# Optimization experiments

Hardware: AMD Instinct MI355X
Metric: run time of the kernel (lower is better)

Reference implementation:

```python
import jax, jax.numpy as jnp
import numpy as np

EPS = 1e-6
DATA_DIM = 2048
LATENT_DIM = 64
ENC = [1024, 1024, 2048]
BATCH = 8192
K_ROUNDS = 24  # fixed proposal rounds for Marsaglia-Tsang rejection (accept prob per round > 0.95)


def _sample_gamma_boosted(key, al, be):
    """Marsaglia-Tsang sampler with alpha-boost, matching the torch al<1 branch.

    Samples Gamma(al+1, 1) via squeeze/rejection, then applies the
    u^(1/al) boost and divides by be, exactly as:
    exp(log(d*v + 1e-6) + log(u + 1e-6)/(al + 1e-6)) / (be + 1e-6)
    """
    d = (al + 1.0) - 1.0 / 3.0              # [B, L]
    c = 1.0 / jnp.sqrt(9.0 * d)             # [B, L]
    k1, k2 = jax.random.split(key)
    eps = jax.random.normal(k1, (K_ROUNDS,) + al.shape, dtype=al.dtype)
    u = jax.random.uniform(k2, (K_ROUNDS,) + al.shape, dtype=al.dtype,
                           minval=1e-7, maxval=1.0)
    v = 1.0 + c[None] * eps                 # [K, B, L]
    v3 = v * v * v
    safe_v3 = jnp.where(v > 0, v3, 1.0)
    # squeeze accept OR full log-accept (standard MT test, as in source index1/index2)
    accept = (v > 0) & ((u < 1.0 - 0.0331 * (eps * eps) * (eps * eps)) |
                        (jnp.log(u) < 0.5 * eps * eps + d[None] * (1.0 - safe_v3 + jnp.log(safe_v3))))
    idx = jnp.argmax(accept, axis=0)        # first accepted round per element
    eps_s = jnp.take_along_axis(eps, idx[None], axis=0)[0]
    u_s = jnp.take_along_axis(u, idx[None], axis=0)[0]
    v_s = (1.0 + c * eps_s) ** 3
    return jnp.exp(jnp.log(d * v_s + EPS) + jnp.log(u_s + EPS) / (al + EPS)) / (be + EPS)


def setup_inputs() -> dict:
    key = jax.random.key(0)
    ks = jax.random.split(key, 20)

    def lin(k, fan_in, fan_out):
        kw, kb = jax.random.split(k)
        w = jax.random.normal(kw, (fan_in, fan_out), dtype=jnp.float32) / np.sqrt(fan_in)
        b = jax.random.normal(kb, (fan_out,), dtype=jnp.float32) * 0.01
        return w, b

    inp = {"x": jax.random.uniform(ks[0], (BATCH, DATA_DIM), dtype=jnp.float32)}
    inp["fc1_w"], inp["fc1_b"] = lin(ks[1], DATA_DIM, ENC[0])
    inp["fc2_w"], inp["fc2_b"] = lin(ks[2], ENC[0], ENC[1])
    inp["fc3_w"], inp["fc3_b"] = lin(ks[3], ENC[1], ENC[2])
    inp["fc41_w"], inp["fc41_b"] = lin(ks[4], ENC[2], LATENT_DIM)
    inp["fc42_w"], inp["fc42_b"] = lin(ks[5], ENC[2], LATENT_DIM)
    inp["fc4_w"], inp["fc4_b"] = lin(ks[6], LATENT_DIM, ENC[2])
    inp["fc5_w"], inp["fc5_b"] = lin(ks[7], ENC[2], ENC[1])
    inp["fc6_w"], inp["fc6_b"] = lin(ks[8], ENC[1], ENC[0])
    inp["fc7_w"], inp["fc7_b"] = lin(ks[9], ENC[0], DATA_DIM * 2)
    return inp


def reference(x, fc1_w, fc1_b, fc2_w, fc2_b, fc3_w, fc3_b,
              fc41_w, fc41_b, fc42_w, fc42_b,
              fc4_w, fc4_b, fc5_w, fc5_b, fc6_w, fc6_b, fc7_w, fc7_b):
    relu, sp = jax.nn.relu, jax.nn.softplus
    # encoder
    h1 = relu(x @ fc1_w + fc1_b)
    h2 = relu(h1 @ fc2_w + fc2_b)
    h3 = relu(h2 @ fc3_w + fc3_b)
    logalpha = EPS + sp(h3 @ fc41_w + fc41_b)   # [B, L], positive
    logbeta = EPS + sp(h3 @ fc42_w + fc42_b)
    # reparameterize via Marsaglia-Tsang gamma rejection sampling
    z = _sample_gamma_boosted(jax.random.key(42), logalpha, logbeta)
    # decoder (torch calls decode(z) twice with identical result; compute once)
    h4 = relu(z @ fc4_w + fc4_b)
    h5 = relu(h4 @ fc5_w + fc5_b)
    h6 = relu(h5 @ fc6_w + fc6_b)
    dec = h6 @ fc7_w + fc7_b                    # [B, 2*DATA_DIM]
    recon_al = EPS + sp(dec[:, :DATA_DIM])
    recon_be = EPS + sp(dec[:, DATA_DIM:])
    return (recon_al, recon_be, logalpha, logbeta, z)
```

## Files before the change

### kernel.cpp

```cpp
#include <hip/hip_runtime.h>
#include <stdint.h>

#define DEVFN static __device__ __forceinline__

typedef __attribute__((ext_vector_type(8))) short short8;
typedef __attribute__((ext_vector_type(4))) float floatx4;
typedef _Float16 half8 __attribute__((ext_vector_type(8)));

DEVFN uint32_t rotl32(uint32_t v, int d) { return (v << d) | (v >> (32 - d)); }

DEVFN void tf2x32(uint32_t k0, uint32_t k1, uint32_t x0, uint32_t x1,
                  uint32_t& o0, uint32_t& o1) {
  uint32_t k2 = k0 ^ k1 ^ 0x1BD11BDAu;
  x0 += k0; x1 += k1;
  x0 += x1; x1 = rotl32(x1, 13); x1 ^= x0;
  x0 += x1; x1 = rotl32(x1, 15); x1 ^= x0;
  x0 += x1; x1 = rotl32(x1, 26); x1 ^= x0;
  x0 += x1; x1 = rotl32(x1, 6);  x1 ^= x0;
  x0 += k1; x1 += k2 + 1u;
  x0 += x1; x1 = rotl32(x1, 17); x1 ^= x0;
  x0 += x1; x1 = rotl32(x1, 29); x1 ^= x0;
  x0 += x1; x1 = rotl32(x1, 16); x1 ^= x0;
  x0 += x1; x1 = rotl32(x1, 24); x1 ^= x0;
  x0 += k2; x1 += k0 + 2u;
  x0 += x1; x1 = rotl32(x1, 13); x1 ^= x0;
  x0 += x1; x1 = rotl32(x1, 15); x1 ^= x0;
  x0 += x1; x1 = rotl32(x1, 26); x1 ^= x0;
  x0 += x1; x1 = rotl32(x1, 6);  x1 ^= x0;
  x0 += k0; x1 += k1 + 3u;
  x0 += x1; x1 = rotl32(x1, 17); x1 ^= x0;
  x0 += x1; x1 = rotl32(x1, 29); x1 ^= x0;
  x0 += x1; x1 = rotl32(x1, 16); x1 ^= x0;
  x0 += x1; x1 = rotl32(x1, 24); x1 ^= x0;
  x0 += k1; x1 += k2 + 4u;
  x0 += x1; x1 = rotl32(x1, 13); x1 ^= x0;
  x0 += x1; x1 = rotl32(x1, 15); x1 ^= x0;
  x0 += x1; x1 = rotl32(x1, 26); x1 ^= x0;
  x0 += x1; x1 = rotl32(x1, 6);  x1 ^= x0;
  x0 += k2; x1 += k0 + 5u;
  o0 = x0; o1 = x1;
}

DEVFN float erfinv_f32(float x) {
#pragma clang fp contract(off)
  float w = -log1pf(-(x * x));
  float p;
  if (w < 5.0f) {
    w = w - 2.5f;
    p = 2.81022636e-08f;
    p = 3.43273939e-07f + p * w;
    p = -3.5233877e-06f + p * w;
    p = -4.39150654e-06f + p * w;
    p = 0.00021858087f + p * w;
    p = -0.00125372503f + p * w;
    p = -0.00417768164f + p * w;
    p = 0.246640727f + p * w;
    p = 1.50140941f + p * w;
  } else {
    w = __fsqrt_rn(w) - 3.0f;
    p = -0.000200214257f;
    p = 0.000100950558f + p * w;
    p = 0.00134934322f + p * w;
    p = -0.00367342844f + p * w;
    p = 0.00573950773f + p * w;
    p = -0.0076224613f + p * w;
    p = 0.00943887047f + p * w;
    p = 1.00167406f + p * w;
    p = 2.83297682f + p * w;
  }
  return p * x;
}

DEVFN float softplus_ref(float v) {
#pragma clang fp contract(off)
  return fmaxf(v, 0.0f) + log1pf(expf(-fabsf(v)));
}

DEVFN float softplus_fast(float v) {
  float e = __expf(-fabsf(v));
  return fmaxf(v, 0.0f) + __logf(1.0f + e);
}

DEVFN ushort f2bf(float f) {
  uint32_t u = __float_as_uint(f);
  uint32_t r = (u + 0x7FFFu + ((u >> 16) & 1u)) >> 16;
  return (ushort)r;
}

DEVFN void split2(float a, ushort& hb, ushort& lb) {
  _Float16 h = (_Float16)a;
  float r = (a - (float)h) * 2048.0f;
  _Float16 l = (_Float16)r;
  hb = __builtin_bit_cast(unsigned short, h);
  lb = __builtin_bit_cast(unsigned short, l);
}

DEVFN void gl2lds16(const void* g, void* l) {
  __builtin_amdgcn_global_load_lds(
      (const __attribute__((address_space(1))) void*)g,
      (__attribute__((address_space(3))) void*)l, 16, 0, 0);
}

DEVFN int xcd_swizzle(int bid, int nwg) {
  if ((nwg & 7) == 0) return (bid & 7) * (nwg >> 3) + (bid >> 3);
  return bid;
}

__global__ __launch_bounds__(256) void split_f16(
    const float* __restrict__ in, ushort* __restrict__ oh,
    ushort* __restrict__ ol, int n4) {
  int idx = blockIdx.x * 256 + threadIdx.x;
  int stride = gridDim.x * 256;
  for (int i = idx; i < n4; i += stride) {
    float4 a = ((const float4*)in)[i];
    ushort h0, h1, h2, h3, l0, l1, l2, l3;
    split2(a.x, h0, l0); split2(a.y, h1, l1);
    split2(a.z, h2, l2); split2(a.w, h3, l3);
    ushort4 hv; hv.x = h0; hv.y = h1; hv.z = h2; hv.w = h3;
    ushort4 lv; lv.x = l0; lv.y = l1; lv.z = l2; lv.w = l3;
    ((ushort4*)oh)[i] = hv;
    ((ushort4*)ol)[i] = lv;
  }
}

__global__ __launch_bounds__(256) void transpose_split_f16(
    const float* __restrict__ in, ushort* __restrict__ oh,
    ushort* __restrict__ ol, int R, int C) {
  __shared__ float tile[32][33];
  const int c0 = blockIdx.x * 32, r0 = blockIdx.y * 32;
  const int tx = threadIdx.x & 31, ty = threadIdx.x >> 5;
#pragma unroll
  for (int i = ty; i < 32; i += 8)
    tile[i][tx] = in[(size_t)(r0 + i) * C + c0 + tx];
  __syncthreads();
#pragma unroll
  for (int i = ty; i < 32; i += 8) {
    ushort hb, lb;
    split2(tile[tx][i], hb, lb);
    size_t o = (size_t)(c0 + i) * R + r0 + tx;
    oh[o] = hb; ol[o] = lb;
  }
}

template <int ACT>
__global__ __launch_bounds__(256) void gemm_f16x3(
    const ushort* __restrict__ Ah, const ushort* __restrict__ Al,
    const ushort* __restrict__ Bh, const ushort* __restrict__ Bl,
    const float* __restrict__ bias, ushort* __restrict__ Oh,
    ushort* __restrict__ Ol, float* __restrict__ Of, int M, int N, int K) {
  __shared__ ushort AsH[2][128 * 32];
  __shared__ ushort AsL[2][128 * 32];
  __shared__ ushort BsH[2][128 * 32];
  __shared__ ushort BsL[2][128 * 32];
  const int tid = threadIdx.x;
  const int wave = tid >> 6, lane = tid & 63;
  const int nbx = gridDim.x;
  const int bid = xcd_swizzle(blockIdx.y * nbx + blockIdx.x, nbx * gridDim.y);
  const int m0 = (bid / nbx) * 128, n0 = (bid % nbx) * 128;
  const int lrow = lane & 15, lq = lane >> 4;
  const int wm = wave & 1, wn = wave >> 1;
  const int srow = lane >> 2;
  const int scol = (lane & 3) * 8;

  floatx4 acc1[4][4], acc2[4][4];
#pragma unroll
  for (int i = 0; i < 4; i++)
#pragma unroll
    for (int j = 0; j < 4; j++) {
      acc1[i][j] = (floatx4){0.f, 0.f, 0.f, 0.f};
      acc2[i][j] = (floatx4){0.f, 0.f, 0.f, 0.f};
    }

  auto stage = [&](int k0, int pp) {
#pragma unroll
    for (int h = 0; h < 2; h++) {
      int r0 = wave * 32 + h * 16;
      gl2lds16(Ah + (size_t)(m0 + r0 + srow) * K + k0 + scol, &AsH[pp][r0 * 32]);
      gl2lds16(Al + (size_t)(m0 + r0 + srow) * K + k0 + scol, &AsL[pp][r0 * 32]);
      gl2lds16(Bh + (size_t)(n0 + r0 + srow) * K + k0 + scol, &BsH[pp][r0 * 32]);
      gl2lds16(Bl + (size_t)(n0 + r0 + srow) * K + k0 + scol, &BsL[pp][r0 * 32]);
    }
  };

  const int nt = K >> 5;
  stage(0, 0);
  int cur = 0;
  for (int t = 0; t < nt; t++) {
    if (t + 1 < nt) {
      stage((t + 1) << 5, cur ^ 1);
      asm volatile("s_waitcnt vmcnt(8)" ::: "memory");
    } else {
      asm volatile("s_waitcnt vmcnt(0)" ::: "memory");
    }
    __builtin_amdgcn_sched_barrier(0);
    __builtin_amdgcn_s_barrier();
    __builtin_amdgcn_sched_barrier(0);
    half8 ah[4], al[4];
#pragma unroll
    for (int i = 0; i < 4; i++) {
      ah[i] = *(const half8*)&AsH[cur][(wm * 64 + i * 16 + lrow) * 32 + lq * 8];
      al[i] = *(const half8*)&AsL[cur][(wm * 64 + i * 16 + lrow) * 32 + lq * 8];
    }
#pragma unroll
    for (int j = 0; j < 4; j++) {
      half8 bh = *(const half8*)&BsH[cur][(wn * 64 + j * 16 + lrow) * 32 + lq * 8];
      half8 bl = *(const half8*)&BsL[cur][(wn * 64 + j * 16 + lrow) * 32 + lq * 8];
#pragma unroll
      for (int i = 0; i < 4; i++) {
        acc1[i][j] = __builtin_amdgcn_mfma_f32_16x16x32_f16(ah[i], bh,
                                                            acc1[i][j], 0, 0, 0);
        acc2[i][j] = __builtin_amdgcn_mfma_f32_16x16x32_f16(ah[i], bl,
                                                            acc2[i][j], 0, 0, 0);
        acc2[i][j] = __builtin_amdgcn_mfma_f32_16x16x32_f16(al[i], bh,
                                                            acc2[i][j], 0, 0, 0);
      }
    }
    __builtin_amdgcn_sched_barrier(0);
    __builtin_amdgcn_s_barrier();
    __builtin_amdgcn_sched_barrier(0);
    cur ^= 1;
  }

  const float INV2048 = 4.8828125e-4f;
#pragma unroll
  for (int i = 0; i < 4; i++) {
#pragma unroll
    for (int j = 0; j < 4; j++) {
      int colg = n0 + wn * 64 + j * 16 + lrow;
      float bb = bias[colg];
#pragma unroll
      for (int r = 0; r < 4; r++) {
        int rowg = m0 + wm * 64 + i * 16 + lq * 4 + r;
        float v = acc1[i][j][r] + acc2[i][j][r] * INV2048 + bb;
        v = fmaxf(v, 0.0f);
        if (ACT == 1) {
          ushort hb, lb;
          split2(v, hb, lb);
          size_t o = (size_t)rowg * N + colg;
          Oh[o] = hb; Ol[o] = lb;
        } else {
          Of[(size_t)rowg * N + colg] = v;
        }
      }
    }
  }
}

__global__ __launch_bounds__(256) void dual_mfma(
    const ushort* __restrict__ Ah, const ushort* __restrict__ Al,
    const ushort* __restrict__ Bh, const ushort* __restrict__ Bl,
    float* __restrict__ P) {
  __shared__ ushort AsH[128 * 32];
  __shared__ ushort AsL[128 * 32];
  __shared__ ushort BsH[128 * 32];
  __shared__ ushort BsL[128 * 32];
  const int K = 2048;
  const int tid = threadIdx.x;
  const int wave = tid >> 6, lane = tid & 63;
  const int m0 = blockIdx.y * 128;
  const int kbase = blockIdx.x * 256;
  const int lrow = lane & 15, lq = lane >> 4;
  const int wm = wave & 1, wn = wave >> 1;
  const int srow = lane >> 2;
  const int scol = (lane & 3) * 8;

  floatx4 acc1[4][4], acc2[4][4];
#pragma unroll
  for (int i = 0; i < 4; i++)
#pragma unroll
    for (int j = 0; j < 4; j++) {
      acc1[i][j] = (floatx4){0.f, 0.f, 0.f, 0.f};
      acc2[i][j] = (floatx4){0.f, 0.f, 0.f, 0.f};
    }

  for (int kk = 0; kk < 256; kk += 32) {
    int k0 = kbase + kk;
#pragma unroll
    for (int h = 0; h < 2; h++) {
      int r0 = wave * 32 + h * 16;
      gl2lds16(Ah + (size_t)(m0 + r0 + srow) * K + k0 + scol, &AsH[r0 * 32]);
      gl2lds16(Al + (size_t)(m0 + r0 + srow) * K + k0 + scol, &AsL[r0 * 32]);
      gl2lds16(Bh + (size_t)(r0 + srow) * K + k0 + scol, &BsH[r0 * 32]);
      gl2lds16(Bl + (size_t)(r0 + srow) * K + k0 + scol, &BsL[r0 * 32]);
    }
    __syncthreads();
    half8 ah[4], al[4];
#pragma unroll
    for (int i = 0; i < 4; i++) {
      ah[i] = *(const half8*)&AsH[(wm * 64 + i * 16 + lrow) * 32 + lq * 8];
      al[i] = *(const half8*)&AsL[(wm * 64 + i * 16 + lrow) * 32 + lq * 8];
    }
#pragma unroll
    for (int j = 0; j < 4; j++) {
      half8 bh = *(const half8*)&BsH[(wn * 64 + j * 16 + lrow) * 32 + lq * 8];
      half8 bl = *(const half8*)&BsL[(wn * 64 + j * 16 + lrow) * 32 + lq * 8];
#pragma unroll
      for (int i = 0; i < 4; i++) {
        acc1[i][j] = __builtin_amdgcn_mfma_f32_16x16x32_f16(ah[i], bh,
                                                            acc1[i][j], 0, 0, 0);
        acc2[i][j] = __builtin_amdgcn_mfma_f32_16x16x32_f16(ah[i], bl,
                                                            acc2[i][j], 0, 0, 0);
        acc2[i][j] = __builtin_amdgcn_mfma_f32_16x16x32_f16(al[i], bh,
                                                            acc2[i][j], 0, 0, 0);
      }
    }
    __syncthreads();
  }

  const float INV2048 = 4.8828125e-4f;
#pragma unroll
  for (int i = 0; i < 4; i++) {
#pragma unroll
    for (int j = 0; j < 4; j++) {
      int colg = wn * 64 + j * 16 + lrow;
#pragma unroll
      for (int r = 0; r < 4; r++) {
        int rowg = m0 + wm * 64 + i * 16 + lq * 4 + r;
        float v = acc1[i][j][r] + acc2[i][j][r] * INV2048;
        P[((size_t)blockIdx.x * 8192 + rowg) * 128 + colg] = v;
      }
    }
  }
}

__global__ __launch_bounds__(256) void dual_reduce(
    const float* __restrict__ P, const float* __restrict__ b41,
    const float* __restrict__ b42, float* __restrict__ la,
    float* __restrict__ lb) {
#pragma clang fp contract(off)
  int idx = blockIdx.x * 256 + threadIdx.x;
  int row = idx >> 5;
  int c4 = (idx & 31) * 4;
  float4 s = {0.f, 0.f, 0.f, 0.f};
#pragma unroll
  for (int k = 0; k < 8; k++) {
    float4 p = *(const float4*)&P[((size_t)k * 8192 + row) * 128 + c4];
    s.x += p.x; s.y += p.y; s.z += p.z; s.w += p.w;
  }
  float o[4];
  const float* bb = (c4 < 64) ? (b41 + c4) : (b42 + c4 - 64);
#pragma unroll
  for (int q = 0; q < 4; q++) {
    float v = (&s.x)[q] + bb[q];
    o[q] = 1e-6f + softplus_ref(v);
  }
  float* dst = (c4 < 64) ? (la + (size_t)row * 64 + c4)
                         : (lb + (size_t)row * 64 + (c4 - 64));
  *(float4*)dst = *(float4*)o;
}

__global__ __launch_bounds__(256) void gamma_sampler(
    const float* __restrict__ la, const float* __restrict__ lb,
    float* __restrict__ z, ushort* __restrict__ zb) {
#pragma clang fp contract(off)
  const uint32_t i = blockIdx.x * 256u + threadIdx.x;
  uint32_t k1a, k1b, k2a, k2b;
  tf2x32(0u, 42u, 0u, 0u, k1a, k1b);
  tf2x32(0u, 42u, 0u, 1u, k2a, k2b);

  const float LO = __uint_as_float(0xBF7FFFFFu);
  const float SQRT2 = __uint_as_float(0x3FB504F3u);
  const float USCALE = 1.0f - 1e-7f;

  const float al = la[i];
  const float be = lb[i];
  const float d = (al + 1.0f) - 0.33333334f;
  const float c = 1.0f / __fsqrt_rn(9.0f * d);

  float es = 0.0f, us = 0.0f;
  bool done = false;
  for (int k = 0; k < 24; k++) {
    if (__all(done)) break;
    if (!done) {
      uint32_t n = (uint32_t)k * 524288u + i;
      uint32_t o0, o1, p0, p1;
      tf2x32(k1a, k1b, 0u, n, o0, o1);
      tf2x32(k2a, k2b, 0u, n, p0, p1);
      uint32_t eb = o0 ^ o1;
      uint32_t ub = p0 ^ p1;
      float f = __uint_as_float((eb >> 9) | 0x3F800000u) - 1.0f;
      float un = f * 2.0f + LO;
      un = fmaxf(LO, un);
      float e = SQRT2 * erfinv_f32(un);
      float g = __uint_as_float((ub >> 9) | 0x3F800000u) - 1.0f;
      float u = g * USCALE + 1e-7f;
      u = fmaxf(1e-7f, u);
      if (k == 0) { es = e; us = u; }
      float v = 1.0f + c * e;
      if (v > 0.0f) {
        float v3 = (v * v) * v;
        float e2 = e * e;
        bool acc = false;
        float sq = 1.0f - (0.0331f * e2) * e2;
        if (u < sq) acc = true;
        else {
          float rhs = (0.5f * e) * e + d * ((1.0f - v3) + logf(v3));
          if (logf(u) < rhs) acc = true;
        }
        if (acc) { es = e; us = u; done = true; }
      }
    }
  }
  float vv = 1.0f + c * es;
  float vs = (vv * vv) * vv;
  float t = logf(d * vs + 1e-6f) + logf(us + 1e-6f) / (al + 1e-6f);
  float zv = expf(t) / (be + 1e-6f);
  z[i] = zv;
  zb[i] = f2bf(zv);
}

__global__ __launch_bounds__(256) void transpose_bf16(
    const float* __restrict__ in, ushort* __restrict__ out, int R, int C) {
  __shared__ float tile[32][33];
  const int c0 = blockIdx.x * 32, r0 = blockIdx.y * 32;
  const int tx = threadIdx.x & 31, ty = threadIdx.x >> 5;
#pragma unroll
  for (int i = ty; i < 32; i += 8)
    tile[i][tx] = in[(size_t)(r0 + i) * C + c0 + tx];
  __syncthreads();
#pragma unroll
  for (int i = ty; i < 32; i += 8)
    out[(size_t)(c0 + i) * R + r0 + tx] = f2bf(tile[tx][i]);
}

template <int ACT>
__global__ __launch_bounds__(256) void gemm_bf16(
    const ushort* __restrict__ A, const ushort* __restrict__ Bt,
    const float* __restrict__ bias, ushort* __restrict__ C0b,
    float* __restrict__ C0f, float* __restrict__ C1f,
    int M, int N, int K, int split) {
  __shared__ ushort As[3][128 * 32];
  __shared__ ushort Bs[3][128 * 32];
  const int tid = threadIdx.x;
  const int wave = tid >> 6, lane = tid & 63;
  const int nbx = gridDim.x;
  const int bid = xcd_swizzle(blockIdx.y * nbx + blockIdx.x, nbx * gridDim.y);
  const int m0 = (bid / nbx) * 128, n0 = (bid % nbx) * 128;
  const int lrow = lane & 15, lq = lane >> 4;
  const int wm = wave & 1, wn = wave >> 1;
  const int srow = lane >> 2;
  const int scol = (lane & 3) * 8;

  floatx4 acc[4][4];
#pragma unroll
  for (int i = 0; i < 4; i++)
#pragma unroll
    for (int j = 0; j < 4; j++) acc[i][j] = (floatx4){0.f, 0.f, 0.f, 0.f};

  auto stage = [&](int k0, int pp) {
#pragma unroll
    for (int h = 0; h < 2; h++) {
      int r0 = wave * 32 + h * 16;
      gl2lds16(A + (size_t)(m0 + r0 + srow) * K + k0 + scol, &As[pp][r0 * 32]);
      gl2lds16(Bt + (size_t)(n0 + r0 + srow) * K + k0 + scol, &Bs[pp][r0 * 32]);
    }
  };

  const int nt = K >> 5;
  stage(0, 0);
  stage(32, 1);
  int cur = 0;
  for (int t = 0; t < nt; t++) {
    if (t + 2 < nt) {
      int nb = cur + 2; if (nb >= 3) nb -= 3;
      stage((t + 2) << 5, nb);
      asm volatile("s_waitcnt vmcnt(8)" ::: "memory");
    } else if (t + 1 < nt) {
      asm volatile("s_waitcnt vmcnt(4)" ::: "memory");
    } else {
      asm volatile("s_waitcnt vmcnt(0)" ::: "memory");
    }
    __builtin_amdgcn_sched_barrier(0);
    __builtin_amdgcn_s_barrier();
    __builtin_amdgcn_sched_barrier(0);
    short8 a[4], b[4];
#pragma unroll
    for (int i = 0; i < 4; i++) {
      a[i] = *(const short8*)&As[cur][(wm * 64 + i * 16 + lrow) * 32 + lq * 8];
      b[i] = *(const short8*)&Bs[cur][(wn * 64 + i * 16 + lrow) * 32 + lq * 8];
    }
#pragma unroll
    for (int i = 0; i < 4; i++)
#pragma unroll
      for (int j = 0; j < 4; j++)
        acc[i][j] = __builtin_amdgcn_mfma_f32_16x16x32_bf16(a[i], b[j],
                                                            acc[i][j], 0, 0, 0);
    __builtin_amdgcn_sched_barrier(0);
    __builtin_amdgcn_s_barrier();
    __builtin_amdgcn_sched_barrier(0);
    cur = cur + 1; if (cur == 3) cur = 0;
  }

#pragma unroll
  for (int i = 0; i < 4; i++) {
#pragma unroll
    for (int j = 0; j < 4; j++) {
      int colg = n0 + wn * 64 + j * 16 + lrow;
      float bb = bias[colg];
#pragma unroll
      for (int r = 0; r < 4; r++) {
        int rowg = m0 + wm * 64 + i * 16 + lq * 4 + r;
        float v = acc[i][j][r] + bb;
        if (ACT == 0) {
          v = fmaxf(v, 0.0f);
          C0b[(size_t)rowg * N + colg] = f2bf(v);
        } else {
          v = 1e-6f + softplus_fast(v);
          if (colg < split) C0f[(size_t)rowg * split + colg] = v;
          else              C1f[(size_t)rowg * split + (colg - split)] = v;
        }
      }
    }
  }
}

extern "C" void kernel_launch(void* const* d_in, const int* in_sizes, int n_in,
                              void* d_out, int out_size, void* d_ws,
                              size_t ws_size, hipStream_t stream) {
  const float* x   = (const float*)d_in[0];
  const float* w1  = (const float*)d_in[1];  const float* b1  = (const float*)d_in[2];
  const float* w2  = (const float*)d_in[3];  const float* b2  = (const float*)d_in[4];
  const float* w3  = (const float*)d_in[5];  const float* b3  = (const float*)d_in[6];
  const float* w41 = (const float*)d_in[7];  const float* b41 = (const float*)d_in[8];
  const float* w42 = (const float*)d_in[9];  const float* b42 = (const float*)d_in[10];
  const float* w4  = (const float*)d_in[11]; const float* b4  = (const float*)d_in[12];
  const float* w5  = (const float*)d_in[13]; const float* b5  = (const float*)d_in[14];
  const float* w6  = (const float*)d_in[15]; const float* b6  = (const float*)d_in[16];
  const float* w7  = (const float*)d_in[17]; const float* b7  = (const float*)d_in[18];
  float* out = (float*)d_out;
  float* ws  = (float*)d_ws;
  ushort* wsu = (ushort*)d_ws;

  float* recon_a = out;
  float* recon_b = out + 16777216;
  float* la      = out + 33554432;
  float* lb      = out + 34078720;
  float* zz      = out + 34603008;

  ushort* xh   = wsu;
  ushort* xl   = wsu + 16777216;
  ushort* w1Th = wsu + 33554432;
  ushort* w1Tl = wsu + 35651584;
  ushort* w2Th = wsu + 37748736;
  ushort* w2Tl = wsu + 38797312;
  ushort* h1h  = wsu + 39845888;
  ushort* h1l  = wsu + 48234496;
  ushort* w3Th = wsu + 16777216;
  ushort* w3Tl = wsu + 18874368;
  ushort* h2h  = wsu;
  ushort* h2l  = wsu + 8388608;
  ushort* h3h  = wsu + 20971520;
  ushort* h3l  = wsu + 37748736;
  ushort* wcatTh = wsu + 16777216;
  ushort* wcatTl = wsu + 17039360;
  float*  Ppart = ws;
  ushort* w4T = wsu + 54525952;
  ushort* w5T = wsu + 54657024;
  ushort* w6T = wsu + 56754176;
  ushort* w7T = wsu + 57802752;
  ushort* zb  = wsu;
  ushort* h4b = wsu + 20971520;
  ushort* h5b = wsu + 524288;
  ushort* h6b = wsu + 8912896;

  dim3 blk(256);
  split_f16<<<dim3(2048), blk, 0, stream>>>(x, xh, xl, 4194304);
  transpose_split_f16<<<dim3(32, 64), blk, 0, stream>>>(w1, w1Th, w1Tl, 2048, 1024);
  transpose_split_f16<<<dim3(32, 32), blk, 0, stream>>>(w2, w2Th, w2Tl, 1024, 1024);
  gemm_f16x3<1><<<dim3(8, 64), blk, 0, stream>>>(xh, xl, w1Th, w1Tl, b1,
                                                 h1h, h1l, nullptr, 8192, 1024, 2048);
  transpose_split_f16<<<dim3(64, 32), blk, 0, stream>>>(w3, w3Th, w3Tl, 1024, 2048);
  gemm_f16x3<1><<<dim3(8, 64), blk, 0, stream>>>(h1h, h1l, w2Th, w2Tl, b2,
                                                 h2h, h2l, nullptr, 8192, 1024, 1024);
  transpose_bf16<<<dim3(64, 2),   blk, 0, stream>>>(w4, w4T, 64,   2048);
  transpose_bf16<<<dim3(32, 64),  blk, 0, stream>>>(w5, w5T, 2048, 1024);
  transpose_bf16<<<dim3(32, 32),  blk, 0, stream>>>(w6, w6T, 1024, 1024);
  transpose_bf16<<<dim3(128, 32), blk, 0, stream>>>(w7, w7T, 1024, 4096);
  gemm_f16x3<1><<<dim3(16, 64), blk, 0, stream>>>(h2h, h2l, w3Th, w3Tl, b3,
                                                  h3h, h3l, nullptr, 8192, 2048, 1024);
  transpose_split_f16<<<dim3(2, 64), blk, 0, stream>>>(w41, wcatTh, wcatTl, 2048, 64);
  transpose_split_f16<<<dim3(2, 64), blk, 0, stream>>>(w42, wcatTh + 64 * 2048,
                                                       wcatTl + 64 * 2048, 2048, 64);
  dual_mfma<<<dim3(8, 64), blk, 0, stream>>>(h3h, h3l, wcatTh, wcatTl, Ppart);
  dual_reduce<<<dim3(1024), blk, 0, stream>>>(Ppart, b41, b42, la, lb);
  gamma_sampler<<<dim3(2048), blk, 0, stream>>>(la, lb, zz, zb);
  gemm_bf16<0><<<dim3(16, 64), blk, 0, stream>>>(zb,  w4T, b4, h4b, nullptr, nullptr, 8192, 2048, 64, 0);
  gemm_bf16<0><<<dim3(8, 64),  blk, 0, stream>>>(h4b, w5T, b5, h5b, nullptr, nullptr, 8192, 1024, 2048, 0);
  gemm_bf16<0><<<dim3(8, 64),  blk, 0, stream>>>(h5b, w6T, b6, h6b, nullptr, nullptr, 8192, 1024, 1024, 0);
  gemm_bf16<3><<<dim3(32, 64), blk, 0, stream>>>(h6b, w7T, b7, nullptr, recon_a, recon_b, 8192, 4096, 1024, 2048);
  (void)in_sizes; (void)n_in; (void)out_size; (void)ws_size;
}
```

Before: 918.0 us.

## Fuse split-K reduction into gamma sampler and use 256x256 tiles for fc7 GEMM

Folds the partial-sum reduction, bias and softplus for logalpha/logbeta into the gamma sampler kernel, which removes one launch and a round trip of la/lb through global memory. zb moves to another workspace offset so it no longer overlaps the Ppart buffer that the sampler now reads. The final 8192x4096x1024 decoder GEMM moves to a new 512-thread kernel with 256x256 tiles and double-buffered LDS, meant to raise operand reuse per block. The larger tile raises register and LDS pressure and cuts the grid to 512 blocks, which may lower occupancy.

```diff
diff --git a/kernel.cpp b/kernel.cpp
--- a/kernel.cpp
+++ b/kernel.cpp
@@ -323,37 +323,24 @@
   }
 }
 
-__global__ __launch_bounds__(256) void dual_reduce(
+__global__ __launch_bounds__(256) void gamma_sampler(
     const float* __restrict__ P, const float* __restrict__ b41,
     const float* __restrict__ b42, float* __restrict__ la,
-    float* __restrict__ lb) {
-#pragma clang fp contract(off)
-  int idx = blockIdx.x * 256 + threadIdx.x;
-  int row = idx >> 5;
-  int c4 = (idx & 31) * 4;
-  float4 s = {0.f, 0.f, 0.f, 0.f};
-#pragma unroll
-  for (int k = 0; k < 8; k++) {
-    float4 p = *(const float4*)&P[((size_t)k * 8192 + row) * 128 + c4];
-    s.x += p.x; s.y += p.y; s.z += p.z; s.w += p.w;
-  }
-  float o[4];
-  const float* bb = (c4 < 64) ? (b41 + c4) : (b42 + c4 - 64);
-#pragma unroll
-  for (int q = 0; q < 4; q++) {
-    float v = (&s.x)[q] + bb[q];
-    o[q] = 1e-6f + softplus_ref(v);
-  }
-  float* dst = (c4 < 64) ? (la + (size_t)row * 64 + c4)
-                         : (lb + (size_t)row * 64 + (c4 - 64));
-  *(float4*)dst = *(float4*)o;
-}
-
-__global__ __launch_bounds__(256) void gamma_sampler(
-    const float* __restrict__ la, const float* __restrict__ lb,
-    float* __restrict__ z, ushort* __restrict__ zb) {
+    float* __restrict__ lb, float* __restrict__ z, ushort* __restrict__ zb) {
 #pragma clang fp contract(off)
   const uint32_t i = blockIdx.x * 256u + threadIdx.x;
+  const int row = i >> 6, col = i & 63;
+  float sa = 0.0f, sb = 0.0f;
+#pragma unroll
+  for (int k = 0; k < 8; k++) {
+    sa += P[((size_t)k * 8192 + row) * 128 + col];
+    sb += P[((size_t)k * 8192 + row) * 128 + 64 + col];
+  }
+  const float al = 1e-6f + softplus_ref(sa + b41[col]);
+  const float be = 1e-6f + softplus_ref(sb + b42[col]);
+  la[i] = al;
+  lb[i] = be;
+
   uint32_t k1a, k1b, k2a, k2b;
   tf2x32(0u, 42u, 0u, 0u, k1a, k1b);
   tf2x32(0u, 42u, 0u, 1u, k2a, k2b);
@@ -362,8 +349,6 @@
   const float SQRT2 = __uint_as_float(0x3FB504F3u);
   const float USCALE = 1.0f - 1e-7f;
 
-  const float al = la[i];
-  const float be = lb[i];
   const float d = (al + 1.0f) - 0.33333334f;
   const float c = 1.0f / __fsqrt_rn(9.0f * d);
 
@@ -514,6 +499,95 @@
   }
 }
 
+template <int ACT>
+__global__ __launch_bounds__(512) void gemm_bf16_256(
+    const ushort* __restrict__ A, const ushort* __restrict__ Bt,
+    const float* __restrict__ bias, ushort* __restrict__ C0b,
+    float* __restrict__ C0f, float* __restrict__ C1f,
+    int M, int N, int K, int split) {
+  __shared__ ushort As[2][256 * 32];
+  __shared__ ushort Bs[2][256 * 32];
+  const int tid = threadIdx.x;
+  const int wave = tid >> 6, lane = tid & 63;
+  const int nbx = gridDim.x;
+  const int bid = xcd_swizzle(blockIdx.y * nbx + blockIdx.x, nbx * gridDim.y);
+  const int m0 = (bid / nbx) * 256, n0 = (bid % nbx) * 256;
+  const int lrow = lane & 15, lq = lane >> 4;
+  const int wm = wave >> 2;
+  const int wnn = wave & 3;
+  const int srow = lane >> 2;
+  const int scol = (lane & 3) * 8;
+
+  floatx4 acc[8][4];
+#pragma unroll
+  for (int i = 0; i < 8; i++)
+#pragma unroll
+    for (int j = 0; j < 4; j++) acc[i][j] = (floatx4){0.f, 0.f, 0.f, 0.f};
+
+  auto stage = [&](int k0, int pp) {
+#pragma unroll
+    for (int h = 0; h < 2; h++) {
+      int r0 = wave * 32 + h * 16;
+      gl2lds16(A + (size_t)(m0 + r0 + srow) * K + k0 + scol, &As[pp][r0 * 32]);
+      gl2lds16(Bt + (size_t)(n0 + r0 + srow) * K + k0 + scol, &Bs[pp][r0 * 32]);
+    }
+  };
+
+  const int nt = K >> 5;
+  stage(0, 0);
+  int cur = 0;
+  for (int t = 0; t < nt; t++) {
+    if (t + 1 < nt) {
+      stage((t + 1) << 5, cur ^ 1);
+      asm volatile("s_waitcnt vmcnt(4)" ::: "memory");
+    } else {
+      asm volatile("s_waitcnt vmcnt(0)" ::: "memory");
+    }
+    __builtin_amdgcn_sched_barrier(0);
+    __builtin_amdgcn_s_barrier();
+    __builtin_amdgcn_sched_barrier(0);
+    short8 a[8], b[4];
+#pragma unroll
+    for (int i = 0; i < 8; i++)
+      a[i] = *(const short8*)&As[cur][(wm * 128 + i * 16 + lrow) * 32 + lq * 8];
+#pragma unroll
+    for (int j = 0; j < 4; j++)
+      b[j] = *(const short8*)&Bs[cur][(wnn * 64 + j * 16 + lrow) * 32 + lq * 8];
+#pragma unroll
+    for (int i = 0; i < 8; i++)
+#pragma unroll
+      for (int j = 0; j < 4; j++)
+        acc[i][j] = __builtin_amdgcn_mfma_f32_16x16x32_bf16(a[i], b[j],
+                                                            acc[i][j], 0, 0, 0);
+    __builtin_amdgcn_sched_barrier(0);
+    __builtin_amdgcn_s_barrier();
+    __builtin_amdgcn_sched_barrier(0);
+    cur ^= 1;
+  }
+
+#pragma unroll
+  for (int i = 0; i < 8; i++) {
+#pragma unroll
+    for (int j = 0; j < 4; j++) {
+      int colg = n0 + wnn * 64 + j * 16 + lrow;
+      float bb = bias[colg];
+#pragma unroll
+      for (int r = 0; r < 4; r++) {
+        int rowg = m0 + wm * 128 + i * 16 + lq * 4 + r;
+        float v = acc[i][j][r] + bb;
+        if (ACT == 0) {
+          v = fmaxf(v, 0.0f);
+          C0b[(size_t)rowg * N + colg] = f2bf(v);
+        } else {
+          v = 1e-6f + softplus_fast(v);
+          if (colg < split) C0f[(size_t)rowg * split + colg] = v;
+          else              C1f[(size_t)rowg * split + (colg - split)] = v;
+        }
+      }
+    }
+  }
+}
+
 extern "C" void kernel_launch(void* const* d_in, const int* in_sizes, int n_in,
                               void* d_out, int out_size, void* d_ws,
                               size_t ws_size, hipStream_t stream) {
@@ -558,7 +632,7 @@
   ushort* w5T = wsu + 54657024;
   ushort* w6T = wsu + 56754176;
   ushort* w7T = wsu + 57802752;
-  ushort* zb  = wsu;
+  ushort* zb  = wsu + 37748736;
   ushort* h4b = wsu + 20971520;
   ushort* h5b = wsu + 524288;
   ushort* h6b = wsu + 8912896;
@@ -582,11 +656,11 @@
   transpose_split_f16<<<dim3(2, 64), blk, 0, stream>>>(w42, wcatTh + 64 * 2048,
                                                        wcatTl + 64 * 2048, 2048, 64);
   dual_mfma<<<dim3(8, 64), blk, 0, stream>>>(h3h, h3l, wcatTh, wcatTl, Ppart);
-  dual_reduce<<<dim3(1024), blk, 0, stream>>>(Ppart, b41, b42, la, lb);
-  gamma_sampler<<<dim3(2048), blk, 0, stream>>>(la, lb, zz, zb);
+  gamma_sampler<<<dim3(2048), blk, 0, stream>>>(Ppart, b41, b42, la, lb, zz, zb);
   gemm_bf16<0><<<dim3(16, 64), blk, 0, stream>>>(zb,  w4T, b4, h4b, nullptr, nullptr, 8192, 2048, 64, 0);
   gemm_bf16<0><<<dim3(8, 64),  blk, 0, stream>>>(h4b, w5T, b5, h5b, nullptr, nullptr, 8192, 1024, 2048, 0);
   gemm_bf16<0><<<dim3(8, 64),  blk, 0, stream>>>(h5b, w6T, b6, h6b, nullptr, nullptr, 8192, 1024, 1024, 0);
-  gemm_bf16<3><<<dim3(32, 64), blk, 0, stream>>>(h6b, w7T, b7, nullptr, recon_a, recon_b, 8192, 4096, 1024, 2048);
+  gemm_bf16_256<3><<<dim3(16, 32), dim3(512), 0, stream>>>(
+      h6b, w7T, b7, nullptr, recon_a, recon_b, 8192, 4096, 1024, 2048);
   (void)in_sizes; (void)n_in; (void)out_size; (void)ws_size;
 }
```

Result: no change. 916.0 us (-0.2%).
